# Performance work log

Measured on AMD Instinct MI355X. Metric: run time of the kernel, lower is better.

Reference implementation:

```python
import jax, jax.numpy as jnp
import numpy as np

N_ATOMS = 8192
N_EDGES = 262144
N_MOL = 128
F = 128
R = 20
CUTOFF = 5.0
L = 3
EPS = 1e-8


def setup_inputs() -> dict:
    key = jax.random.key(0)
    ks = jax.random.split(key, 20)
    sc = 0.05  # weight init scale for numerical stability
    inp = {
        "z": jax.random.randint(ks[0], (N_ATOMS,), 0, 100, dtype=jnp.int32),
        "pos": jax.random.uniform(ks[1], (N_ATOMS, 3), dtype=jnp.float32),
        "edge_src": jax.random.randint(ks[2], (N_EDGES,), 0, N_ATOMS, dtype=jnp.int32),
        "edge_dst": jax.random.randint(ks[3], (N_EDGES,), 0, N_ATOMS, dtype=jnp.int32),
        "mol_idx": jnp.sort(jax.random.randint(ks[4], (N_ATOMS,), 0, N_MOL, dtype=jnp.int32)),
        "embed": jax.random.normal(ks[5], (100, F), dtype=jnp.float32) * sc,
        "msg_w1": jax.random.normal(ks[6], (L, F, F), dtype=jnp.float32) * sc,
        "msg_b1": jnp.zeros((L, F), jnp.float32),
        "msg_w2": jax.random.normal(ks[7], (L, F, 3 * F), dtype=jnp.float32) * sc,
        "msg_b2": jnp.zeros((L, 3 * F), jnp.float32),
        "rbf_w": jax.random.normal(ks[8], (L, R, 3 * F), dtype=jnp.float32) * sc,
        "rbf_b": jnp.zeros((L, 3 * F), jnp.float32),
        "upd_u": jax.random.normal(ks[9], (L, F, F), dtype=jnp.float32) * sc,
        "upd_v": jax.random.normal(ks[10], (L, F, F), dtype=jnp.float32) * sc,
        "upd_a1": jax.random.normal(ks[11], (L, 2 * F, F), dtype=jnp.float32) * sc,
        "upd_a1b": jnp.zeros((L, F), jnp.float32),
        "upd_a2": jax.random.normal(ks[12], (L, F, 3 * F), dtype=jnp.float32) * sc,
        "upd_a2b": jnp.zeros((L, 3 * F), jnp.float32),
        "out_w1": jax.random.normal(ks[13], (F, F), dtype=jnp.float32) * sc,
        "out_b1": jnp.zeros((F,), jnp.float32),
        "out_w2": jax.random.normal(ks[14], (F, 1), dtype=jnp.float32) * sc,
        "out_b2": jnp.zeros((1,), jnp.float32),
    }
    return inp


def _painn_forward(z, pos, edge_src, edge_dst, mol_idx, embed,
                   msg_w1, msg_b1, msg_w2, msg_b2, rbf_w, rbf_b,
                   upd_u, upd_v, upd_a1, upd_a1b, upd_a2, upd_a2b,
                   out_w1, out_b1, out_w2, out_b2):
    n = z.shape[0]
    s = embed[z]                                  # [N,F]
    v = jnp.zeros((n, 3, F), s.dtype)             # [N,3,F]

    rij = pos[edge_dst] - pos[edge_src]           # [E,3]
    d = jnp.sqrt(jnp.sum(rij * rij, axis=-1) + EPS)  # [E]
    unit = rij / d[:, None]                       # [E,3]
    freq = jnp.arange(1, R + 1, dtype=s.dtype) * (jnp.pi / CUTOFF)
    rbf = jnp.sin(d[:, None] * freq[None, :]) / d[:, None]          # [E,R]
    fc = 0.5 * (jnp.cos(jnp.pi * d / CUTOFF) + 1.0) * (d < CUTOFF)  # [E]

    for l in range(L):
        # --- message block ---
        phi = jax.nn.silu(s @ msg_w1[l] + msg_b1[l]) @ msg_w2[l] + msg_b2[l]  # [N,3F]
        wfilt = (rbf @ rbf_w[l] + rbf_b[l]) * fc[:, None]                      # [E,3F]
        m = phi[edge_src] * wfilt                                              # [E,3F]
        ds_e, dvv, dvs = m[:, :F], m[:, F:2 * F], m[:, 2 * F:]
        ds = jax.ops.segment_sum(ds_e, edge_dst, num_segments=n)
        dv_e = v[edge_src] * dvv[:, None, :] + unit[:, :, None] * dvs[:, None, :]  # [E,3,F]
        dv = jax.ops.segment_sum(dv_e, edge_dst, num_segments=n)
        s = s + ds
        v = v + dv
        # --- update block ---
        uv = jnp.einsum('ncf,fg->ncg', v, upd_u[l])   # [N,3,F]
        vv = jnp.einsum('ncf,fg->ncg', v, upd_v[l])   # [N,3,F]
        vv_norm = jnp.sqrt(jnp.sum(vv * vv, axis=1) + EPS)  # [N,F]
        a = jax.nn.silu(jnp.concatenate([s, vv_norm], axis=-1) @ upd_a1[l] + upd_a1b[l])
        a = a @ upd_a2[l] + upd_a2b[l]                # [N,3F]
        a_vv, a_sv, a_ss = a[:, :F], a[:, F:2 * F], a[:, 2 * F:]
        s = s + a_ss + a_sv * jnp.sum(uv * vv, axis=1)
        v = v + a_vv[:, None, :] * uv

    atom_out = jax.nn.silu(s @ out_w1 + out_b1) @ out_w2 + out_b2  # [N,1]
    return jax.ops.segment_sum(atom_out, mol_idx, num_segments=N_MOL)  # [M,1]


def reference(z, pos, edge_src, edge_dst, mol_idx, embed,
              msg_w1, msg_b1, msg_w2, msg_b2, rbf_w, rbf_b,
              upd_u, upd_v, upd_a1, upd_a1b, upd_a2, upd_a2b,
              out_w1, out_b1, out_w2, out_b2):
    return _painn_forward(z, pos, edge_src, edge_dst, mol_idx, embed,
                          msg_w1, msg_b1, msg_w2, msg_b2, rbf_w, rbf_b,
                          upd_u, upd_v, upd_a1, upd_a1b, upd_a2, upd_a2b,
                          out_w1, out_b1, out_w2, out_b2)
```

## Files before the change

### kernel.cpp

```cpp
#include <hip/hip_runtime.h>
#include <hip/hip_bf16.h>
#include <math.h>

#define N_ATOMS 8192
#define N_EDGES 262144
#define N_MOL   128
#define FDIM    128
#define RDIM    20
#define LLAYERS 3
#define CUTOFF  5.0f
#define EPSV    1e-8f
#define PI_F    3.14159265358979323846f

typedef __attribute__((ext_vector_type(8))) short bf16x8;
typedef __attribute__((ext_vector_type(4))) float f32x4;

#define VPLANE 1048576

__device__ __forceinline__ ushort f2bf(float x) {
    uint b = __float_as_uint(x);
    return (ushort)((b + 0x7fffu + ((b >> 16) & 1u)) >> 16);
}

__global__ void k_wconv(const float* __restrict__ w1, const float* __restrict__ w2,
                        const float* __restrict__ uu, const float* __restrict__ uvw,
                        const float* __restrict__ a1, const float* __restrict__ a2,
                        const float* __restrict__ ow1, ushort* __restrict__ WT) {
    int i = blockIdx.x * 256 + threadIdx.x;
    float v;
    if (i < 49152) {
        int idx = i; int l = idx >> 14; idx &= 16383;
        int n = idx >> 7, k = idx & 127;
        v = w1[l*16384 + k*128 + n];
    } else if (i < 196608) {
        int idx = i - 49152; int l = idx / 49152; idx -= l * 49152;
        int n = idx >> 7, k = idx & 127;
        v = w2[l*49152 + k*384 + n];
    } else if (i < 294912) {
        int idx = i - 196608; int l = idx >> 15; idx &= 32767;
        int n = idx >> 7, k = idx & 127;
        v = (n < 128) ? uu[l*16384 + k*128 + n] : uvw[l*16384 + k*128 + (n-128)];
    } else if (i < 393216) {
        int idx = i - 294912; int l = idx >> 15; idx &= 32767;
        int n = idx >> 8, k = idx & 255;
        v = a1[l*32768 + k*128 + n];
    } else if (i < 540672) {
        int idx = i - 393216; int l = idx / 49152; idx -= l * 49152;
        int n = idx >> 7, k = idx & 127;
        v = a2[l*49152 + k*384 + n];
    } else {
        int idx = i - 540672;
        int n = idx >> 7, k = idx & 127;
        v = ow1[k*128 + n];
    }
    WT[i] = f2bf(v);
}

__global__ void k_embed(const int* __restrict__ z, const float* __restrict__ embed,
                        float* __restrict__ S, ushort* __restrict__ SBF) {
    int i = blockIdx.x * 256 + threadIdx.x;
    int a = i >> 7, k = i & 127;
    float v = embed[(size_t)z[a] * FDIM + k];
    S[i] = v; SBF[i] = f2bf(v);
}

__global__ void k_hist(const int* __restrict__ edst, int* __restrict__ CNT) {
    int e = blockIdx.x * 256 + threadIdx.x;
    if (e < N_EDGES) atomicAdd(&CNT[edst[e]], 1);
}

__global__ __launch_bounds__(1024) void k_scan(const int* __restrict__ CNT,
                                               int* __restrict__ OFF, int* __restrict__ CUR) {
    __shared__ int part[1024];
    int t = threadIdx.x;
    int loc[8];
    int run = 0;
    #pragma unroll
    for (int i = 0; i < 8; i++) { int c = CNT[t*8 + i]; loc[i] = run; run += c; }
    part[t] = run;
    __syncthreads();
    for (int off = 1; off < 1024; off <<= 1) {
        int v = 0;
        if (t >= off) v = part[t - off];
        __syncthreads();
        part[t] += v;
        __syncthreads();
    }
    int ebase = (t > 0) ? part[t-1] : 0;
    #pragma unroll
    for (int i = 0; i < 8; i++) { int o = ebase + loc[i]; OFF[t*8+i] = o; CUR[t*8+i] = o; }
    if (t == 1023) OFF[8192] = part[1023];
}

__global__ void k_edges(const float* __restrict__ pos, const int* __restrict__ esrc,
                        const int* __restrict__ edst, int* __restrict__ CUR,
                        float* __restrict__ RBF, float* __restrict__ UNITFC,
                        int* __restrict__ SRCS) {
    int e = blockIdx.x * 256 + threadIdx.x;
    if (e >= N_EDGES) return;
    int s = esrc[e], d = edst[e];
    int p = atomicAdd(&CUR[d], 1);
    float rx = pos[d*3+0] - pos[s*3+0];
    float ry = pos[d*3+1] - pos[s*3+1];
    float rz = pos[d*3+2] - pos[s*3+2];
    float dd = sqrtf(rx*rx + ry*ry + rz*rz + EPSV);
    float inv = 1.0f / dd;
    float fc = (dd < CUTOFF) ? 0.5f * (cosf(dd * (PI_F / CUTOFF)) + 1.0f) : 0.0f;
    float4 u4; u4.x = rx*inv; u4.y = ry*inv; u4.z = rz*inv; u4.w = fc;
    *(float4*)&UNITFC[(size_t)p*4] = u4;
    SRCS[p] = s;
    float rb[RDIM];
    #pragma unroll
    for (int r = 0; r < RDIM; r++) {
        float freq = (float)(r + 1) * (PI_F / CUTOFF);
        rb[r] = sinf(dd * freq) * inv;
    }
    float4* out = (float4*)&RBF[(size_t)p * RDIM];
    #pragma unroll
    for (int q = 0; q < 5; q++) {
        float4 o; o.x = rb[q*4]; o.y = rb[q*4+1]; o.z = rb[q*4+2]; o.w = rb[q*4+3];
        out[q] = o;
    }
}

__global__ __launch_bounds__(256) void k_msg(
    const ushort* __restrict__ SBF, const ushort* __restrict__ W1T, const float* __restrict__ b1,
    const ushort* __restrict__ W2T, const float* __restrict__ b2, ushort* __restrict__ PHIB)
{
    int tid = threadIdx.x;
    int w = tid >> 6, l = tid & 63;
    int bm = blockIdx.x * 16;
    int lrow = l & 15, lk = (l >> 4) * 8;
    __shared__ ushort Hs[16][136];

    f32x4 acc[2] = {{0.f,0.f,0.f,0.f},{0.f,0.f,0.f,0.f}};
    #pragma unroll
    for (int k0 = 0; k0 < 128; k0 += 32) {
        bf16x8 af = *(const bf16x8*)&SBF[(size_t)(bm + lrow)*128 + k0 + lk];
        #pragma unroll
        for (int t = 0; t < 2; t++) {
            int n = (2*w + t)*16 + lrow;
            bf16x8 bf = *(const bf16x8*)&W1T[(size_t)n*128 + k0 + lk];
            acc[t] = __builtin_amdgcn_mfma_f32_16x16x32_bf16(af, bf, acc[t], 0, 0, 0);
        }
    }
    #pragma unroll
    for (int t = 0; t < 2; t++) {
        int col = (2*w + t)*16 + lrow;
        float bv = b1[col];
        #pragma unroll
        for (int j = 0; j < 4; j++) {
            int row = (l >> 4)*4 + j;
            float val = acc[t][j] + bv;
            val = val / (1.0f + __expf(-val));
            Hs[row][col] = f2bf(val);
        }
    }
    __syncthreads();

    f32x4 acc2[6];
    #pragma unroll
    for (int t = 0; t < 6; t++) acc2[t] = (f32x4){0.f,0.f,0.f,0.f};
    #pragma unroll
    for (int k0 = 0; k0 < 128; k0 += 32) {
        bf16x8 af = *(const bf16x8*)&Hs[lrow][k0 + lk];
        #pragma unroll
        for (int t = 0; t < 6; t++) {
            int n = (6*w + t)*16 + lrow;
            bf16x8 bf = *(const bf16x8*)&W2T[(size_t)n*128 + k0 + lk];
            acc2[t] = __builtin_amdgcn_mfma_f32_16x16x32_bf16(af, bf, acc2[t], 0, 0, 0);
        }
    }
    #pragma unroll
    for (int t = 0; t < 6; t++) {
        int col = (6*w + t)*16 + lrow;
        float bv = b2[col];
        #pragma unroll
        for (int j = 0; j < 4; j++) {
            int row = bm + (l >> 4)*4 + j;
            PHIB[(size_t)row*384 + col] = f2bf(acc2[t][j] + bv);
        }
    }
}

template<bool L0>
__global__ __launch_bounds__(192) void k_aggregate(
    const ushort* __restrict__ PHIB, const ushort* __restrict__ VBFA,
    float* __restrict__ S, ushort* __restrict__ SBF,
    float* __restrict__ V, ushort* __restrict__ VBFB,
    const float* __restrict__ RBF, const float* __restrict__ UNITFC,
    const int* __restrict__ SRCS, const int* __restrict__ OFF,
    const float* __restrict__ rbfw, const float* __restrict__ rbfb)
{
    int tid = threadIdx.x;
    int g = tid >> 6;
    int c0 = 2 * (tid & 63);

    float2 w[RDIM];
    const float* wc = rbfw + g*128 + c0;
    #pragma unroll
    for (int r = 0; r < RDIM; r++) { w[r].x = wc[r*384]; w[r].y = wc[r*384 + 1]; }
    float2 bb; bb.x = rbfb[g*128 + c0]; bb.y = rbfb[g*128 + c0 + 1];

    __shared__ int sSrc[64];
    __shared__ float4 sRBF[320];
    __shared__ float4 sUFC[64];
    __shared__ float avs[3][128];

    for (int ai = 0; ai < 4; ai++) {
        int a = blockIdx.x * 4 + ai;
        int beg = OFF[a], end = OFF[a + 1];
        float2 d; d.x = 0.f; d.y = 0.f;
        float2 A0, A1, A2v;
        A0.x=A0.y=A1.x=A1.y=A2v.x=A2v.y=0.f;

        for (int p0 = beg; p0 < end; p0 += 64) {
            int n = end - p0; if (n > 64) n = 64;
            __syncthreads();
            if (tid < n) sSrc[tid] = SRCS[p0 + tid];
            for (int i = tid; i < n; i += 192)
                sUFC[i] = *(const float4*)(UNITFC + (size_t)(p0 + i) * 4);
            {
                const float4* rsrc = (const float4*)(RBF + (size_t)p0 * RDIM);
                for (int i = tid; i < n*5; i += 192) sRBF[i] = rsrc[i];
            }
            __syncthreads();

            if (L0 && g == 1) continue;

            uint phA[4], u0A[4], u1A[4], u2A[4];
            uint phB[4], u0B[4], u1B[4], u2B[4];

            auto grpLoad = [&](int base, uint* ph, uint* u0, uint* u1, uint* u2) {
                #pragma unroll
                for (int j = 0; j < 4; j++) {
                    int q = base + j;
                    int src = sSrc[(q < n) ? q : 0];
                    size_t pb = (size_t)src * 128;
                    ph[j] = *(const uint*)&PHIB[(size_t)src*384 + g*128 + c0];
                    if (!L0 && g == 1) {
                        u0[j] = *(const uint*)&VBFA[pb + c0];
                        u1[j] = *(const uint*)&VBFA[pb + VPLANE + c0];
                        u2[j] = *(const uint*)&VBFA[pb + 2*VPLANE + c0];
                    }
                }
            };
            grpLoad(0, phA, u0A, u1A, u2A);
            for (int q0 = 0; q0 < n; q0 += 4) {
                if (q0 + 4 < n) grpLoad(q0 + 4, phB, u0B, u1B, u2B);
                #pragma unroll
                for (int j = 0; j < 4; j++) {
                    int q = q0 + j;
                    if (q >= n) break;
                    float4 r0 = sRBF[q*5+0], r1 = sRBF[q*5+1], r2 = sRBF[q*5+2],
                           r3 = sRBF[q*5+3], r4 = sRBF[q*5+4];
                    float4 ufc = sUFC[q];
                    float2 f = bb;
                    f.x += r0.x*w[0].x;   f.y += r0.x*w[0].y;
                    f.x += r0.y*w[1].x;   f.y += r0.y*w[1].y;
                    f.x += r0.z*w[2].x;   f.y += r0.z*w[2].y;
                    f.x += r0.w*w[3].x;   f.y += r0.w*w[3].y;
                    f.x += r1.x*w[4].x;   f.y += r1.x*w[4].y;
                    f.x += r1.y*w[5].x;   f.y += r1.y*w[5].y;
                    f.x += r1.z*w[6].x;   f.y += r1.z*w[6].y;
                    f.x += r1.w*w[7].x;   f.y += r1.w*w[7].y;
                    f.x += r2.x*w[8].x;   f.y += r2.x*w[8].y;
                    f.x += r2.y*w[9].x;   f.y += r2.y*w[9].y;
                    f.x += r2.z*w[10].x;  f.y += r2.z*w[10].y;
                    f.x += r2.w*w[11].x;  f.y += r2.w*w[11].y;
                    f.x += r3.x*w[12].x;  f.y += r3.x*w[12].y;
                    f.x += r3.y*w[13].x;  f.y += r3.y*w[13].y;
                    f.x += r3.z*w[14].x;  f.y += r3.z*w[14].y;
                    f.x += r3.w*w[15].x;  f.y += r3.w*w[15].y;
                    f.x += r4.x*w[16].x;  f.y += r4.x*w[16].y;
                    f.x += r4.y*w[17].x;  f.y += r4.y*w[17].y;
                    f.x += r4.z*w[18].x;  f.y += r4.z*w[18].y;
                    f.x += r4.w*w[19].x;  f.y += r4.w*w[19].y;
                    uint up = phA[j];
                    float m0 = __uint_as_float(up << 16)         * (f.x * ufc.w);
                    float m1 = __uint_as_float(up & 0xffff0000u) * (f.y * ufc.w);
                    if (g == 0) {
                        d.x += m0; d.y += m1;
                    } else if (g == 1) {
                        A0.x  += __uint_as_float(u0A[j] << 16)         * m0;
                        A0.y  += __uint_as_float(u0A[j] & 0xffff0000u) * m1;
                        A1.x  += __uint_as_float(u1A[j] << 16)         * m0;
                        A1.y  += __uint_as_float(u1A[j] & 0xffff0000u) * m1;
                        A2v.x += __uint_as_float(u2A[j] << 16)         * m0;
                        A2v.y += __uint_as_float(u2A[j] & 0xffff0000u) * m1;
                    } else {
                        A0.x  += ufc.x * m0; A0.y  += ufc.x * m1;
                        A1.x  += ufc.y * m0; A1.y  += ufc.y * m1;
                        A2v.x += ufc.z * m0; A2v.y += ufc.z * m1;
                    }
                }
                #pragma unroll
                for (int j = 0; j < 4; j++) {
                    phA[j] = phB[j]; u0A[j] = u0B[j]; u1A[j] = u1B[j]; u2A[j] = u2B[j];
                }
            }
        }

        if (g == 1) {
            avs[0][c0] = A0.x;  avs[0][c0+1] = A0.y;
            avs[1][c0] = A1.x;  avs[1][c0+1] = A1.y;
            avs[2][c0] = A2v.x; avs[2][c0+1] = A2v.y;
        }
        __syncthreads();
        if (g == 0) {
            size_t sb = (size_t)a*128 + c0;
            float2 s2 = *(float2*)&S[sb];
            s2.x += d.x; s2.y += d.y;
            *(float2*)&S[sb] = s2;
            SBF[sb] = f2bf(s2.x); SBF[sb+1] = f2bf(s2.y);
        } else if (g == 2) {
            float own0[3] = {A0.x, A1.x, A2v.x};
            float own1[3] = {A0.y, A1.y, A2v.y};
            #pragma unroll
            for (int c = 0; c < 3; c++) {
                size_t vb = (size_t)c*VPLANE + (size_t)a*128 + c0;
                float2 vi;
                if (L0) { vi.x = 0.f; vi.y = 0.f; }
                else    vi = *(const float2*)&V[vb];
                vi.x += avs[c][c0]     + own0[c];
                vi.y += avs[c][c0 + 1] + own1[c];
                *(float2*)&V[vb] = vi;
                VBFB[vb] = f2bf(vi.x); VBFB[vb+1] = f2bf(vi.y);
            }
        }
    }
}

__global__ __launch_bounds__(256) void k_upd(
    const ushort* __restrict__ VBFB, const ushort* __restrict__ UVT,
    const ushort* __restrict__ SBF_in,
    const ushort* __restrict__ A1T, const float* __restrict__ a1b,
    const ushort* __restrict__ A2T, const float* __restrict__ a2b,
    float* __restrict__ S, ushort* __restrict__ SBF,
    float* __restrict__ V, ushort* __restrict__ VBFA)
{
    int tid = threadIdx.x;
    int w = tid >> 6, l = tid & 63;
    int bm = blockIdx.x * 16;
    int lrow = l & 15, lk = (l >> 4) * 8;
    __shared__ ushort sVVN[16][136];
    __shared__ ushort Hs[16][136];

    f32x4 au[3][2], av[3][2];
    #pragma unroll
    for (int c = 0; c < 3; c++)
        #pragma unroll
        for (int t = 0; t < 2; t++) {
            au[c][t] = (f32x4){0.f,0.f,0.f,0.f};
            av[c][t] = (f32x4){0.f,0.f,0.f,0.f};
        }
    #pragma unroll
    for (int k0 = 0; k0 < 128; k0 += 32) {
        bf16x8 af[3];
        #pragma unroll
        for (int c = 0; c < 3; c++)
            af[c] = *(const bf16x8*)&VBFB[(size_t)c*VPLANE + (size_t)(bm + lrow)*128 + k0 + lk];
        #pragma unroll
        for (int t = 0; t < 2; t++) {
            int nu = (2*w + t)*16 + lrow;
            bf16x8 bu = *(const bf16x8*)&UVT[(size_t)nu*128 + k0 + lk];
            bf16x8 bv = *(const bf16x8*)&UVT[(size_t)(nu + 128)*128 + k0 + lk];
            #pragma unroll
            for (int c = 0; c < 3; c++) {
                au[c][t] = __builtin_amdgcn_mfma_f32_16x16x32_bf16(af[c], bu, au[c][t], 0, 0, 0);
                av[c][t] = __builtin_amdgcn_mfma_f32_16x16x32_bf16(af[c], bv, av[c][t], 0, 0, 0);
            }
        }
    }
    float dotr[2][4], uvr[3][2][4];
    #pragma unroll
    for (int t = 0; t < 2; t++) {
        int k = (2*w + t)*16 + lrow;
        #pragma unroll
        for (int j = 0; j < 4; j++) {
            int row = (l >> 4)*4 + j;
            float u0 = au[0][t][j], u1 = au[1][t][j], u2 = au[2][t][j];
            float v0 = av[0][t][j], v1 = av[1][t][j], v2 = av[2][t][j];
            uvr[0][t][j] = u0; uvr[1][t][j] = u1; uvr[2][t][j] = u2;
            dotr[t][j] = u0*v0 + u1*v1 + u2*v2;
            sVVN[row][k] = f2bf(sqrtf(v0*v0 + v1*v1 + v2*v2 + EPSV));
        }
    }
    __syncthreads();

    f32x4 acc[2] = {{0.f,0.f,0.f,0.f},{0.f,0.f,0.f,0.f}};
    #pragma unroll
    for (int k0 = 0; k0 < 256; k0 += 32) {
        bf16x8 af;
        if (k0 < 128) af = *(const bf16x8*)&SBF_in[(size_t)(bm + lrow)*128 + k0 + lk];
        else          af = *(const bf16x8*)&sVVN[lrow][k0 + lk - 128];
        #pragma unroll
        for (int t = 0; t < 2; t++) {
            int n = (2*w + t)*16 + lrow;
            bf16x8 bf = *(const bf16x8*)&A1T[(size_t)n*256 + k0 + lk];
            acc[t] = __builtin_amdgcn_mfma_f32_16x16x32_bf16(af, bf, acc[t], 0, 0, 0);
        }
    }
    #pragma unroll
    for (int t = 0; t < 2; t++) {
        int col = (2*w + t)*16 + lrow;
        float bv = a1b[col];
        #pragma unroll
        for (int j = 0; j < 4; j++) {
            int row = (l >> 4)*4 + j;
            float val = acc[t][j] + bv;
            val = val / (1.0f + __expf(-val));
            Hs[row][col] = f2bf(val);
        }
    }
    __syncthreads();

    f32x4 c_vv[2], c_sv[2], c_ss[2];
    #pragma unroll
    for (int t = 0; t < 2; t++) {
        c_vv[t] = (f32x4){0.f,0.f,0.f,0.f};
        c_sv[t] = (f32x4){0.f,0.f,0.f,0.f};
        c_ss[t] = (f32x4){0.f,0.f,0.f,0.f};
    }
    #pragma unroll
    for (int k0 = 0; k0 < 128; k0 += 32) {
        bf16x8 af = *(const bf16x8*)&Hs[lrow][k0 + lk];
        #pragma unroll
        for (int t = 0; t < 2; t++) {
            int n0 = (2*w + t)*16 + lrow;
            bf16x8 b0 = *(const bf16x8*)&A2T[(size_t)n0*128 + k0 + lk];
            bf16x8 b1 = *(const bf16x8*)&A2T[(size_t)(n0 + 128)*128 + k0 + lk];
            bf16x8 b2 = *(const bf16x8*)&A2T[(size_t)(n0 + 256)*128 + k0 + lk];
            c_vv[t] = __builtin_amdgcn_mfma_f32_16x16x32_bf16(af, b0, c_vv[t], 0, 0, 0);
            c_sv[t] = __builtin_amdgcn_mfma_f32_16x16x32_bf16(af, b1, c_sv[t], 0, 0, 0);
            c_ss[t] = __builtin_amdgcn_mfma_f32_16x16x32_bf16(af, b2, c_ss[t], 0, 0, 0);
        }
    }
    #pragma unroll
    for (int t = 0; t < 2; t++) {
        int k = (2*w + t)*16 + lrow;
        float b_vv = a2b[k], b_sv = a2b[128 + k], b_ss = a2b[256 + k];
        #pragma unroll
        for (int j = 0; j < 4; j++) {
            int a = bm + (l >> 4)*4 + j;
            size_t base = (size_t)a*128 + k;
            float vv = c_vv[t][j] + b_vv;
            float sv = c_sv[t][j] + b_sv;
            float ss = c_ss[t][j] + b_ss;
            float sn = S[base] + ss + sv * dotr[t][j];
            S[base] = sn; SBF[base] = f2bf(sn);
            #pragma unroll
            for (int c = 0; c < 3; c++) {
                size_t vb = (size_t)c*VPLANE + base;
                float nv = V[vb] + vv * uvr[c][t][j];
                V[vb] = nv; VBFA[vb] = f2bf(nv);
            }
        }
    }
}

__global__ __launch_bounds__(64) void k_readout(
    const ushort* __restrict__ SBF, const ushort* __restrict__ OW1T,
    const float* __restrict__ b1, const float* __restrict__ w2,
    const float* __restrict__ b2v, const int* __restrict__ mol,
    float* __restrict__ out)
{
    int l = threadIdx.x;
    int bm = blockIdx.x * 16;
    int lrow = l & 15, lk = (l >> 4) * 8;
    __shared__ float Hs[16][132];

    f32x4 acc[8];
    #pragma unroll
    for (int t = 0; t < 8; t++) acc[t] = (f32x4){0.f,0.f,0.f,0.f};
    #pragma unroll
    for (int k0 = 0; k0 < 128; k0 += 32) {
        bf16x8 af = *(const bf16x8*)&SBF[(size_t)(bm + lrow)*128 + k0 + lk];
        #pragma unroll
        for (int t = 0; t < 8; t++) {
            bf16x8 bf = *(const bf16x8*)&OW1T[(size_t)(t*16 + lrow)*128 + k0 + lk];
            acc[t] = __builtin_amdgcn_mfma_f32_16x16x32_bf16(af, bf, acc[t], 0, 0, 0);
        }
    }
    #pragma unroll
    for (int t = 0; t < 8; t++) {
        int col = t*16 + lrow;
        float bv = b1[col];
        #pragma unroll
        for (int j = 0; j < 4; j++) {
            int row = (l >> 4)*4 + j;
            float val = acc[t][j] + bv;
            Hs[row][col] = val / (1.0f + __expf(-val));
        }
    }
    __syncthreads();
    if (l < 16) {
        float s = b2v[0];
        #pragma unroll 8
        for (int k = 0; k < 128; k++) s += Hs[l][k] * w2[k];
        atomicAdd(&out[mol[bm + l]], s);
    }
}

extern "C" void kernel_launch(void* const* d_in, const int* in_sizes, int n_in,
                              void* d_out, int out_size, void* d_ws, size_t ws_size,
                              hipStream_t stream) {
    const int*   z      = (const int*)d_in[0];
    const float* pos    = (const float*)d_in[1];
    const int*   esrc   = (const int*)d_in[2];
    const int*   edst   = (const int*)d_in[3];
    const int*   mol    = (const int*)d_in[4];
    const float* embed  = (const float*)d_in[5];
    const float* msg_w1 = (const float*)d_in[6];
    const float* msg_b1 = (const float*)d_in[7];
    const float* msg_w2 = (const float*)d_in[8];
    const float* msg_b2 = (const float*)d_in[9];
    const float* rbf_w  = (const float*)d_in[10];
    const float* rbf_b  = (const float*)d_in[11];
    const float* upd_u  = (const float*)d_in[12];
    const float* upd_v  = (const float*)d_in[13];
    const float* upd_a1 = (const float*)d_in[14];
    const float* upd_a1b= (const float*)d_in[15];
    const float* upd_a2 = (const float*)d_in[16];
    const float* upd_a2b= (const float*)d_in[17];
    const float* out_w1 = (const float*)d_in[18];
    const float* out_b1 = (const float*)d_in[19];
    const float* out_w2 = (const float*)d_in[20];
    const float* out_b2 = (const float*)d_in[21];

    float* ws = (float*)d_ws;
    float* S      = ws; ws += 1048576;
    float* V      = ws; ws += 3145728;
    float* RBF    = ws; ws += 5242880;
    float* UNITFC = ws; ws += 1048576;
    ushort* PHIB  = (ushort*)ws; ws += 1572864;
    ushort* VBFA  = (ushort*)ws; ws += 1572864;
    ushort* VBFB  = (ushort*)ws; ws += 1572864;
    ushort* SBF   = (ushort*)ws; ws += 524288;
    ushort* WT    = (ushort*)ws; ws += 278528;
    int* CNT  = (int*)ws;
    int* OFF  = CNT + 8192;
    int* CUR  = OFF + 8193;
    int* SRCS = CUR + 8192;

    hipMemsetAsync(CNT, 0, 8192 * sizeof(int), stream);
    hipMemsetAsync(d_out, 0, N_MOL * sizeof(float), stream);

    k_wconv<<<2176, 256, 0, stream>>>(msg_w1, msg_w2, upd_u, upd_v, upd_a1, upd_a2, out_w1, WT);
    k_embed<<<4096, 256, 0, stream>>>(z, embed, S, SBF);
    k_hist<<<1024, 256, 0, stream>>>(edst, CNT);
    k_scan<<<1, 1024, 0, stream>>>(CNT, OFF, CUR);
    k_edges<<<1024, 256, 0, stream>>>(pos, esrc, edst, CUR, RBF, UNITFC, SRCS);

    for (int l = 0; l < LLAYERS; l++) {
        const ushort* W1T = WT + l*16384;
        const ushort* W2T = WT + 49152  + l*49152;
        const ushort* UVT = WT + 196608 + l*32768;
        const ushort* A1T = WT + 294912 + l*32768;
        const ushort* A2T = WT + 393216 + l*49152;

        k_msg<<<512, 256, 0, stream>>>(SBF, W1T, msg_b1 + (size_t)l*128,
                                       W2T, msg_b2 + (size_t)l*384, PHIB);
        if (l == 0)
            k_aggregate<true><<<2048, 192, 0, stream>>>(PHIB, VBFA, S, SBF, V, VBFB,
                RBF, UNITFC, SRCS, OFF, rbf_w + (size_t)l*20*384, rbf_b + (size_t)l*384);
        else
            k_aggregate<false><<<2048, 192, 0, stream>>>(PHIB, VBFA, S, SBF, V, VBFB,
                RBF, UNITFC, SRCS, OFF, rbf_w + (size_t)l*20*384, rbf_b + (size_t)l*384);
        k_upd<<<512, 256, 0, stream>>>(VBFB, UVT, SBF, A1T, upd_a1b + (size_t)l*128,
            A2T, upd_a2b + (size_t)l*384, S, SBF, V, VBFA);
    }

    k_readout<<<512, 64, 0, stream>>>(SBF, WT + 540672, out_b1, out_w2, out_b2,
                                      mol, (float*)d_out);
}
```

Baseline: 654.8 us.

## Recompute radial basis in aggregate kernel and launch one block per atom

The edge kernel no longer writes a 20-float radial basis per edge. It stores only the distance in the w slot of UNITFC, and each aggregate block recomputes the sin basis and cosine cutoff into shared memory with fast intrinsics. This removes a roughly 20 MB buffer write and its re-read in each of the three layers, at the cost of extra transcendental work repeated per layer. The aggregate kernel also moves from four atoms per block to one atom per block, giving four times as many blocks and fewer serial iterations per block. The __sinf/__cosf intrinsics trade some accuracy for speed.

Measured after the change: 603.1 us. 1.09x faster.

```diff
diff --git a/kernel.cpp b/kernel.cpp
--- a/kernel.cpp
+++ b/kernel.cpp
@@ -94,8 +94,7 @@
 
 __global__ void k_edges(const float* __restrict__ pos, const int* __restrict__ esrc,
                         const int* __restrict__ edst, int* __restrict__ CUR,
-                        float* __restrict__ RBF, float* __restrict__ UNITFC,
-                        int* __restrict__ SRCS) {
+                        float* __restrict__ UNITFC, int* __restrict__ SRCS) {
     int e = blockIdx.x * 256 + threadIdx.x;
     if (e >= N_EDGES) return;
     int s = esrc[e], d = edst[e];
@@ -105,22 +104,9 @@
     float rz = pos[d*3+2] - pos[s*3+2];
     float dd = sqrtf(rx*rx + ry*ry + rz*rz + EPSV);
     float inv = 1.0f / dd;
-    float fc = (dd < CUTOFF) ? 0.5f * (cosf(dd * (PI_F / CUTOFF)) + 1.0f) : 0.0f;
-    float4 u4; u4.x = rx*inv; u4.y = ry*inv; u4.z = rz*inv; u4.w = fc;
+    float4 u4; u4.x = rx*inv; u4.y = ry*inv; u4.z = rz*inv; u4.w = dd;
     *(float4*)&UNITFC[(size_t)p*4] = u4;
     SRCS[p] = s;
-    float rb[RDIM];
-    #pragma unroll
-    for (int r = 0; r < RDIM; r++) {
-        float freq = (float)(r + 1) * (PI_F / CUTOFF);
-        rb[r] = sinf(dd * freq) * inv;
-    }
-    float4* out = (float4*)&RBF[(size_t)p * RDIM];
-    #pragma unroll
-    for (int q = 0; q < 5; q++) {
-        float4 o; o.x = rb[q*4]; o.y = rb[q*4+1]; o.z = rb[q*4+2]; o.w = rb[q*4+3];
-        out[q] = o;
-    }
 }
 
 __global__ __launch_bounds__(256) void k_msg(
@@ -188,10 +174,11 @@
     const ushort* __restrict__ PHIB, const ushort* __restrict__ VBFA,
     float* __restrict__ S, ushort* __restrict__ SBF,
     float* __restrict__ V, ushort* __restrict__ VBFB,
-    const float* __restrict__ RBF, const float* __restrict__ UNITFC,
+    const float* __restrict__ UNITFC,
     const int* __restrict__ SRCS, const int* __restrict__ OFF,
     const float* __restrict__ rbfw, const float* __restrict__ rbfb)
 {
+    int a = blockIdx.x;
     int tid = threadIdx.x;
     int g = tid >> 6;
     int c0 = 2 * (tid & 63);
@@ -206,127 +193,130 @@
     __shared__ float4 sRBF[320];
     __shared__ float4 sUFC[64];
     __shared__ float avs[3][128];
-
-    for (int ai = 0; ai < 4; ai++) {
-        int a = blockIdx.x * 4 + ai;
-        int beg = OFF[a], end = OFF[a + 1];
-        float2 d; d.x = 0.f; d.y = 0.f;
-        float2 A0, A1, A2v;
-        A0.x=A0.y=A1.x=A1.y=A2v.x=A2v.y=0.f;
-
-        for (int p0 = beg; p0 < end; p0 += 64) {
-            int n = end - p0; if (n > 64) n = 64;
-            __syncthreads();
-            if (tid < n) sSrc[tid] = SRCS[p0 + tid];
-            for (int i = tid; i < n; i += 192)
-                sUFC[i] = *(const float4*)(UNITFC + (size_t)(p0 + i) * 4);
-            {
-                const float4* rsrc = (const float4*)(RBF + (size_t)p0 * RDIM);
-                for (int i = tid; i < n*5; i += 192) sRBF[i] = rsrc[i];
-            }
-            __syncthreads();
-
-            if (L0 && g == 1) continue;
-
-            uint phA[4], u0A[4], u1A[4], u2A[4];
-            uint phB[4], u0B[4], u1B[4], u2B[4];
-
-            auto grpLoad = [&](int base, uint* ph, uint* u0, uint* u1, uint* u2) {
-                #pragma unroll
-                for (int j = 0; j < 4; j++) {
-                    int q = base + j;
-                    int src = sSrc[(q < n) ? q : 0];
-                    size_t pb = (size_t)src * 128;
-                    ph[j] = *(const uint*)&PHIB[(size_t)src*384 + g*128 + c0];
-                    if (!L0 && g == 1) {
-                        u0[j] = *(const uint*)&VBFA[pb + c0];
-                        u1[j] = *(const uint*)&VBFA[pb + VPLANE + c0];
-                        u2[j] = *(const uint*)&VBFA[pb + 2*VPLANE + c0];
-                    }
-                }
-            };
-            grpLoad(0, phA, u0A, u1A, u2A);
-            for (int q0 = 0; q0 < n; q0 += 4) {
-                if (q0 + 4 < n) grpLoad(q0 + 4, phB, u0B, u1B, u2B);
-                #pragma unroll
-                for (int j = 0; j < 4; j++) {
-                    int q = q0 + j;
-                    if (q >= n) break;
-                    float4 r0 = sRBF[q*5+0], r1 = sRBF[q*5+1], r2 = sRBF[q*5+2],
-                           r3 = sRBF[q*5+3], r4 = sRBF[q*5+4];
-                    float4 ufc = sUFC[q];
-                    float2 f = bb;
-                    f.x += r0.x*w[0].x;   f.y += r0.x*w[0].y;
-                    f.x += r0.y*w[1].x;   f.y += r0.y*w[1].y;
-                    f.x += r0.z*w[2].x;   f.y += r0.z*w[2].y;
-                    f.x += r0.w*w[3].x;   f.y += r0.w*w[3].y;
-                    f.x += r1.x*w[4].x;   f.y += r1.x*w[4].y;
-                    f.x += r1.y*w[5].x;   f.y += r1.y*w[5].y;
-                    f.x += r1.z*w[6].x;   f.y += r1.z*w[6].y;
-                    f.x += r1.w*w[7].x;   f.y += r1.w*w[7].y;
-                    f.x += r2.x*w[8].x;   f.y += r2.x*w[8].y;
-                    f.x += r2.y*w[9].x;   f.y += r2.y*w[9].y;
-                    f.x += r2.z*w[10].x;  f.y += r2.z*w[10].y;
-                    f.x += r2.w*w[11].x;  f.y += r2.w*w[11].y;
-                    f.x += r3.x*w[12].x;  f.y += r3.x*w[12].y;
-                    f.x += r3.y*w[13].x;  f.y += r3.y*w[13].y;
-                    f.x += r3.z*w[14].x;  f.y += r3.z*w[14].y;
-                    f.x += r3.w*w[15].x;  f.y += r3.w*w[15].y;
-                    f.x += r4.x*w[16].x;  f.y += r4.x*w[16].y;
-                    f.x += r4.y*w[17].x;  f.y += r4.y*w[17].y;
-                    f.x += r4.z*w[18].x;  f.y += r4.z*w[18].y;
-                    f.x += r4.w*w[19].x;  f.y += r4.w*w[19].y;
-                    uint up = phA[j];
-                    float m0 = __uint_as_float(up << 16)         * (f.x * ufc.w);
-                    float m1 = __uint_as_float(up & 0xffff0000u) * (f.y * ufc.w);
-                    if (g == 0) {
-                        d.x += m0; d.y += m1;
-                    } else if (g == 1) {
-                        A0.x  += __uint_as_float(u0A[j] << 16)         * m0;
-                        A0.y  += __uint_as_float(u0A[j] & 0xffff0000u) * m1;
-                        A1.x  += __uint_as_float(u1A[j] << 16)         * m0;
-                        A1.y  += __uint_as_float(u1A[j] & 0xffff0000u) * m1;
-                        A2v.x += __uint_as_float(u2A[j] << 16)         * m0;
-                        A2v.y += __uint_as_float(u2A[j] & 0xffff0000u) * m1;
-                    } else {
-                        A0.x  += ufc.x * m0; A0.y  += ufc.x * m1;
-                        A1.x  += ufc.y * m0; A1.y  += ufc.y * m1;
-                        A2v.x += ufc.z * m0; A2v.y += ufc.z * m1;
-                    }
-                }
-                #pragma unroll
-                for (int j = 0; j < 4; j++) {
-                    phA[j] = phB[j]; u0A[j] = u0B[j]; u1A[j] = u1B[j]; u2A[j] = u2B[j];
+    float* sRBFf = (float*)sRBF;
+
+    int beg = OFF[a], end = OFF[a + 1];
+    float2 d; d.x = 0.f; d.y = 0.f;
+    float2 A0, A1, A2v;
+    A0.x=A0.y=A1.x=A1.y=A2v.x=A2v.y=0.f;
+
+    for (int p0 = beg; p0 < end; p0 += 64) {
+        int n = end - p0; if (n > 64) n = 64;
+        __syncthreads();
+        if (tid < n) {
+            sSrc[tid] = SRCS[p0 + tid];
+            float4 u4 = *(const float4*)(UNITFC + (size_t)(p0 + tid) * 4);
+            float dd = u4.w;
+            u4.w = (dd < CUTOFF) ? 0.5f * (__cosf(dd * (PI_F / CUTOFF)) + 1.0f) : 0.0f;
+            sUFC[tid] = u4;
+        }
+        for (int i = tid; i < n * RDIM; i += 192) {
+            int e = i / RDIM, r = i - e * RDIM;
+            float dd = UNITFC[(size_t)(p0 + e) * 4 + 3];
+            sRBFf[i] = __sinf(dd * (float)(r + 1) * (PI_F / CUTOFF)) / dd;
+        }
+        __syncthreads();
+
+        if (L0 && g == 1) continue;
+
+        uint phA[4], u0A[4], u1A[4], u2A[4];
+        uint phB[4], u0B[4], u1B[4], u2B[4];
+
+        auto grpLoad = [&](int base, uint* ph, uint* u0, uint* u1, uint* u2) {
+            #pragma unroll
+            for (int j = 0; j < 4; j++) {
+                int q = base + j;
+                int src = sSrc[(q < n) ? q : 0];
+                size_t pb = (size_t)src * 128;
+                ph[j] = *(const uint*)&PHIB[(size_t)src*384 + g*128 + c0];
+                if (!L0 && g == 1) {
+                    u0[j] = *(const uint*)&VBFA[pb + c0];
+                    u1[j] = *(const uint*)&VBFA[pb + VPLANE + c0];
+                    u2[j] = *(const uint*)&VBFA[pb + 2*VPLANE + c0];
                 }
             }
-        }
-
-        if (g == 1) {
-            avs[0][c0] = A0.x;  avs[0][c0+1] = A0.y;
-            avs[1][c0] = A1.x;  avs[1][c0+1] = A1.y;
-            avs[2][c0] = A2v.x; avs[2][c0+1] = A2v.y;
-        }
-        __syncthreads();
-        if (g == 0) {
-            size_t sb = (size_t)a*128 + c0;
-            float2 s2 = *(float2*)&S[sb];
-            s2.x += d.x; s2.y += d.y;
-            *(float2*)&S[sb] = s2;
-            SBF[sb] = f2bf(s2.x); SBF[sb+1] = f2bf(s2.y);
-        } else if (g == 2) {
-            float own0[3] = {A0.x, A1.x, A2v.x};
-            float own1[3] = {A0.y, A1.y, A2v.y};
+        };
+        grpLoad(0, phA, u0A, u1A, u2A);
+        for (int q0 = 0; q0 < n; q0 += 4) {
+            if (q0 + 4 < n) grpLoad(q0 + 4, phB, u0B, u1B, u2B);
             #pragma unroll
-            for (int c = 0; c < 3; c++) {
-                size_t vb = (size_t)c*VPLANE + (size_t)a*128 + c0;
-                float2 vi;
-                if (L0) { vi.x = 0.f; vi.y = 0.f; }
-                else    vi = *(const float2*)&V[vb];
-                vi.x += avs[c][c0]     + own0[c];
-                vi.y += avs[c][c0 + 1] + own1[c];
-                *(float2*)&V[vb] = vi;
-                VBFB[vb] = f2bf(vi.x); VBFB[vb+1] = f2bf(vi.y);
+            for (int j = 0; j < 4; j++) {
+                int q = q0 + j;
+                if (q >= n) break;
+                float4 r0 = sRBF[q*5+0], r1 = sRBF[q*5+1], r2 = sRBF[q*5+2],
+                       r3 = sRBF[q*5+3], r4 = sRBF[q*5+4];
+                float4 ufc = sUFC[q];
+                float2 f = bb;
+                f.x += r0.x*w[0].x;   f.y += r0.x*w[0].y;
+                f.x += r0.y*w[1].x;   f.y += r0.y*w[1].y;
+                f.x += r0.z*w[2].x;   f.y += r0.z*w[2].y;
+                f.x += r0.w*w[3].x;   f.y += r0.w*w[3].y;
+                f.x += r1.x*w[4].x;   f.y += r1.x*w[4].y;
+                f.x += r1.y*w[5].x;   f.y += r1.y*w[5].y;
+                f.x += r1.z*w[6].x;   f.y += r1.z*w[6].y;
+                f.x += r1.w*w[7].x;   f.y += r1.w*w[7].y;
+                f.x += r2.x*w[8].x;   f.y += r2.x*w[8].y;
+                f.x += r2.y*w[9].x;   f.y += r2.y*w[9].y;
+                f.x += r2.z*w[10].x;  f.y += r2.z*w[10].y;
+                f.x += r2.w*w[11].x;  f.y += r2.w*w[11].y;
+                f.x += r3.x*w[12].x;  f.y += r3.x*w[12].y;
+                f.x += r3.y*w[13].x;  f.y += r3.y*w[13].y;
+                f.x += r3.z*w[14].x;  f.y += r3.z*w[14].y;
+                f.x += r3.w*w[15].x;  f.y += r3.w*w[15].y;
+                f.x += r4.x*w[16].x;  f.y += r4.x*w[16].y;
+                f.x += r4.y*w[17].x;  f.y += r4.y*w[17].y;
+                f.x += r4.z*w[18].x;  f.y += r4.z*w[18].y;
+                f.x += r4.w*w[19].x;  f.y += r4.w*w[19].y;
+                uint up = phA[j];
+                float m0 = __uint_as_float(up << 16)         * (f.x * ufc.w);
+                float m1 = __uint_as_float(up & 0xffff0000u) * (f.y * ufc.w);
+                if (g == 0) {
+                    d.x += m0; d.y += m1;
+                } else if (g == 1) {
+                    A0.x  += __uint_as_float(u0A[j] << 16)         * m0;
+                    A0.y  += __uint_as_float(u0A[j] & 0xffff0000u) * m1;
+                    A1.x  += __uint_as_float(u1A[j] << 16)         * m0;
+                    A1.y  += __uint_as_float(u1A[j] & 0xffff0000u) * m1;
+                    A2v.x += __uint_as_float(u2A[j] << 16)         * m0;
+                    A2v.y += __uint_as_float(u2A[j] & 0xffff0000u) * m1;
+                } else {
+                    A0.x  += ufc.x * m0; A0.y  += ufc.x * m1;
+                    A1.x  += ufc.y * m0; A1.y  += ufc.y * m1;
+                    A2v.x += ufc.z * m0; A2v.y += ufc.z * m1;
+                }
             }
+            #pragma unroll
+            for (int j = 0; j < 4; j++) {
+                phA[j] = phB[j]; u0A[j] = u0B[j]; u1A[j] = u1B[j]; u2A[j] = u2B[j];
+            }
+        }
+    }
+
+    if (g == 1) {
+        avs[0][c0] = A0.x;  avs[0][c0+1] = A0.y;
+        avs[1][c0] = A1.x;  avs[1][c0+1] = A1.y;
+        avs[2][c0] = A2v.x; avs[2][c0+1] = A2v.y;
+    }
+    __syncthreads();
+    if (g == 0) {
+        size_t sb = (size_t)a*128 + c0;
+        float2 s2 = *(float2*)&S[sb];
+        s2.x += d.x; s2.y += d.y;
+        *(float2*)&S[sb] = s2;
+        SBF[sb] = f2bf(s2.x); SBF[sb+1] = f2bf(s2.y);
+    } else if (g == 2) {
+        float own0[3] = {A0.x, A1.x, A2v.x};
+        float own1[3] = {A0.y, A1.y, A2v.y};
+        #pragma unroll
+        for (int c = 0; c < 3; c++) {
+            size_t vb = (size_t)c*VPLANE + (size_t)a*128 + c0;
+            float2 vi;
+            if (L0) { vi.x = 0.f; vi.y = 0.f; }
+            else    vi = *(const float2*)&V[vb];
+            vi.x += avs[c][c0]     + own0[c];
+            vi.y += avs[c][c0 + 1] + own1[c];
+            *(float2*)&V[vb] = vi;
+            VBFB[vb] = f2bf(vi.x); VBFB[vb+1] = f2bf(vi.y);
         }
     }
 }
@@ -531,7 +521,6 @@
     float* ws = (float*)d_ws;
     float* S      = ws; ws += 1048576;
     float* V      = ws; ws += 3145728;
-    float* RBF    = ws; ws += 5242880;
     float* UNITFC = ws; ws += 1048576;
     ushort* PHIB  = (ushort*)ws; ws += 1572864;
     ushort* VBFA  = (ushort*)ws; ws += 1572864;
@@ -550,7 +539,7 @@
     k_embed<<<4096, 256, 0, stream>>>(z, embed, S, SBF);
     k_hist<<<1024, 256, 0, stream>>>(edst, CNT);
     k_scan<<<1, 1024, 0, stream>>>(CNT, OFF, CUR);
-    k_edges<<<1024, 256, 0, stream>>>(pos, esrc, edst, CUR, RBF, UNITFC, SRCS);
+    k_edges<<<1024, 256, 0, stream>>>(pos, esrc, edst, CUR, UNITFC, SRCS);
 
     for (int l = 0; l < LLAYERS; l++) {
         const ushort* W1T = WT + l*16384;
@@ -562,11 +551,11 @@
         k_msg<<<512, 256, 0, stream>>>(SBF, W1T, msg_b1 + (size_t)l*128,
                                        W2T, msg_b2 + (size_t)l*384, PHIB);
         if (l == 0)
-            k_aggregate<true><<<2048, 192, 0, stream>>>(PHIB, VBFA, S, SBF, V, VBFB,
-                RBF, UNITFC, SRCS, OFF, rbf_w + (size_t)l*20*384, rbf_b + (size_t)l*384);
+            k_aggregate<true><<<8192, 192, 0, stream>>>(PHIB, VBFA, S, SBF, V, VBFB,
+                UNITFC, SRCS, OFF, rbf_w + (size_t)l*20*384, rbf_b + (size_t)l*384);
         else
-            k_aggregate<false><<<2048, 192, 0, stream>>>(PHIB, VBFA, S, SBF, V, VBFB,
-                RBF, UNITFC, SRCS, OFF, rbf_w + (size_t)l*20*384, rbf_b + (size_t)l*384);
+            k_aggregate<false><<<8192, 192, 0, stream>>>(PHIB, VBFA, S, SBF, V, VBFB,
+                UNITFC, SRCS, OFF, rbf_w + (size_t)l*20*384, rbf_b + (size_t)l*384);
         k_upd<<<512, 256, 0, stream>>>(VBFB, UVT, SBF, A1T, upd_a1b + (size_t)l*128,
             A2T, upd_a2b + (size_t)l*384, S, SBF, V, VBFA);
     }
```
